# Kernel optimization log

Measured on AMD Instinct MI355X. Metric: run time of the kernel, lower is better.

## Reference

```python
import jax, jax.numpy as jnp
import numpy as np

B, S, D, H = 4, 2048, 1024, 16
HD = D // H
EPS = 1e-5


def setup_inputs() -> dict:
    key = jax.random.key(0)
    ks = jax.random.split(key, 12)
    scale = 1.0 / np.sqrt(D)
    inp = {
        "x": jax.random.normal(ks[0], (B, S, D), dtype=jnp.float32),
        "template_ids": jax.random.randint(ks[1], (B, S), 0, 1000, dtype=jnp.int64)
            if jax.config.jax_enable_x64 else jax.random.randint(ks[1], (B, S), 0, 1000, dtype=jnp.int32),
        "attention_mask": jnp.ones((B, S), dtype=jnp.int32),
        "Wq": jax.random.normal(ks[2], (D, D), dtype=jnp.float32) * scale,
        "bq": jnp.zeros((D,), dtype=jnp.float32),
        "Wk": jax.random.normal(ks[3], (D, D), dtype=jnp.float32) * scale,
        "bk": jnp.zeros((D,), dtype=jnp.float32),
        "Wv": jax.random.normal(ks[4], (D, D), dtype=jnp.float32) * scale,
        "bv": jnp.zeros((D,), dtype=jnp.float32),
        "Wo": jax.random.normal(ks[5], (D, D), dtype=jnp.float32) * scale,
        "bo": jnp.zeros((D,), dtype=jnp.float32),
        "gamma": jnp.ones((D,), dtype=jnp.float32),
        "beta": jnp.zeros((D,), dtype=jnp.float32),
    }
    return inp


def _split_heads(t):
    # [B,S,D] -> [B,H,S,HD]
    return t.reshape(B, S, H, HD).transpose(0, 2, 1, 3)


def reference(x, template_ids, attention_mask, Wq, bq, Wk, bk, Wv, bv, Wo, bo, gamma, beta):
    q = _split_heads(x @ Wq.T + bq)
    k = _split_heads(x @ Wk.T + bk)
    v = _split_heads(x @ Wv.T + bv)
    # [B,H,S,S]
    scores = jnp.einsum("bhqd,bhkd->bhqk", q, k) / jnp.sqrt(jnp.float32(HD))
    mask = attention_mask[:, None, None, :]  # broadcast over heads and query dim
    scores = jnp.where(mask == 0, jnp.float32(-10000.0), scores)
    attn = jax.nn.softmax(scores, axis=-1)  # dropout is identity in eval
    out = jnp.einsum("bhqk,bhkd->bhqd", attn, v)
    out = out.transpose(0, 2, 1, 3).reshape(B, S, D)
    out = out @ Wo.T + bo
    # residual + LayerNorm
    y = x + out
    mu = jnp.mean(y, axis=-1, keepdims=True)
    var = jnp.var(y, axis=-1, keepdims=True)
    return (y - mu) * jax.lax.rsqrt(var + EPS) * gamma + beta
```

## Files before the change

kernel.cpp:

```cpp
#include <hip/hip_runtime.h>

typedef unsigned short u16;
typedef unsigned int u32;
typedef __attribute__((ext_vector_type(8))) short bf16x8;
typedef __attribute__((ext_vector_type(4))) float f32x4;

#define NB 4
#define SS 2048
#define DD 1024
#define NH 16
#define HD 64
#define MM (NB*SS)

struct __align__(16) Pack16 { unsigned int w0, w1, w2, w3; };
union PU { Pack16 p; u16 s[8]; };

__device__ __forceinline__ float b2f(u16 u) {
    union { unsigned int i; float f; } v; v.i = ((unsigned int)u) << 16; return v.f;
}
__device__ __forceinline__ u16 f2b(float f) {
    union { unsigned int i; float f; } v; v.f = f;
    return (u16)((v.i + 0x7FFFu + ((v.i >> 16) & 1u)) >> 16);
}
__device__ __forceinline__ float rdS(const void* p, size_t i, int mode) {
    return mode ? ((const float*)p)[i] : b2f(((const u16*)p)[i]);
}
__device__ __forceinline__ float ex2(float x) { return __builtin_amdgcn_exp2f(x); }
__device__ __forceinline__ u32 cvtpk(float lo, float hi) {
    u32 r;
    asm("v_cvt_pk_bf16_f32 %0, %1, %2" : "=v"(r) : "v"(lo), "v"(hi));
    return r;
}

__device__ __forceinline__ void cp16(const u16* g, u16* l) {
    __builtin_amdgcn_global_load_lds(
        (const __attribute__((address_space(1))) void*)g,
        (__attribute__((address_space(3))) void*)l, 16, 0, 0);
}

__device__ __forceinline__ void pl32swap(u32& a, u32& b) {
    asm volatile("v_permlane32_swap_b32 %0, %1" : "+v"(a), "+v"(b));
}
__device__ __forceinline__ void pl16swap(u32& a, u32& b) {
    asm volatile("v_permlane16_swap_b32 %0, %1" : "+v"(a), "+v"(b));
}

#define QSC 0.1803368801111204f
#define GX ((size_t)MM * DD / 8)
#define GW ((size_t)DD * DD / 8)
#define GTOT (GX + 4 * GW + 512)

__global__ __launch_bounds__(256) void convert_kernel(
    const void* __restrict__ x,
    const void* __restrict__ Wq, const void* __restrict__ Wk,
    const void* __restrict__ Wv, const void* __restrict__ Wo,
    const void* __restrict__ bq, const void* __restrict__ bk,
    const void* __restrict__ bv, const void* __restrict__ bo,
    u16* __restrict__ xb, u16* __restrict__ Wc, u16* __restrict__ Wob,
    u16* __restrict__ bcat, const u32* __restrict__ gamma_w)
{
    const int mode = (gamma_w[0] == 0x3F800000u) ? 1 : 0;
    size_t g = (size_t)blockIdx.x * 256 + threadIdx.x;
    const void* src; u16* dst; size_t off; float sc = 1.0f;
    if (g < GX)               { src = x;  dst = xb;              off = g * 8; }
    else if (g < GX + GW)     { src = Wq; dst = Wc;              off = (g - GX) * 8; sc = QSC; }
    else if (g < GX + 2 * GW) { src = Wk; dst = Wc + (size_t)DD * DD;     off = (g - GX - GW) * 8; }
    else if (g < GX + 3 * GW) { src = Wv; dst = Wc + (size_t)2 * DD * DD; off = (g - GX - 2 * GW) * 8; }
    else if (g < GX + 4 * GW) { src = Wo; dst = Wob;             off = (g - GX - 3 * GW) * 8; }
    else {
        size_t gg = g - (GX + 4 * GW);
        int which = (int)(gg >> 7); off = (gg & 127) * 8;
        src = (which == 0) ? bq : (which == 1) ? bk : (which == 2) ? bv : bo;
        dst = bcat + which * DD;
        if (which == 0) sc = QSC;
    }
    PU o;
    if (mode) {
        const float* s = (const float*)src + off;
        float4 a = ((const float4*)s)[0];
        float4 b = ((const float4*)s)[1];
        o.s[0] = f2b(a.x * sc); o.s[1] = f2b(a.y * sc);
        o.s[2] = f2b(a.z * sc); o.s[3] = f2b(a.w * sc);
        o.s[4] = f2b(b.x * sc); o.s[5] = f2b(b.y * sc);
        o.s[6] = f2b(b.z * sc); o.s[7] = f2b(b.w * sc);
    } else {
        PU in; in.p = *(const Pack16*)((const u16*)src + off);
#pragma unroll
        for (int j = 0; j < 8; j++) o.s[j] = f2b(b2f(in.s[j]) * sc);
    }
    *(Pack16*)(dst + off) = o.p;
}

__global__ __launch_bounds__(256) void gemm_qkv(
    const u16* __restrict__ xb, const u16* __restrict__ Wc, const u16* __restrict__ bcat,
    u16* __restrict__ Q, u16* __restrict__ K, u16* __restrict__ V)
{
    __shared__ __align__(16) u16 sh[2 * 128 * 64];
    u16* As = sh;
    u16* Bs = sh + 128 * 64;

    const int lin = blockIdx.x;
    const int xcd = lin & 7;
    const int loc = lin >> 3;
    const int m0 = (xcd * 8 + (loc & 7)) * 128;
    const int n0 = (loc >> 3) * 128;

    const int tid  = threadIdx.x;
    const int wv   = tid >> 6;
    const int lane = tid & 63;
    const int wy = wv >> 1, wx = wv & 1;
    const int l15 = lane & 15, quad = lane >> 4;
    const int srow = lane >> 3;
    const int sw   = ((lane & 7) ^ srow) * 8;
    const int key  = l15 & 7;

    f32x4 acc[4][4];
#pragma unroll
    for (int i = 0; i < 4; i++)
#pragma unroll
        for (int j = 0; j < 4; j++) acc[i][j] = (f32x4){0.f, 0.f, 0.f, 0.f};

    for (int k0 = 0; k0 < DD; k0 += 64) {
#pragma unroll
        for (int c = 0; c < 4; c++) {
            cp16(&xb[(size_t)(m0 + wv * 32 + c * 8 + srow) * DD + k0 + sw],
                 &As[wv * 2048 + c * 512]);
            cp16(&Wc[(size_t)(n0 + wv * 32 + c * 8 + srow) * DD + k0 + sw],
                 &Bs[wv * 2048 + c * 512]);
        }
        __syncthreads();
#pragma unroll
        for (int ks = 0; ks < 2; ks++) {
            bf16x8 a[4], bb[4];
#pragma unroll
            for (int mt = 0; mt < 4; mt++)
                a[mt] = *(const bf16x8*)&As[(wy * 64 + mt * 16 + l15) * 64 +
                                            (((ks << 2) + quad) ^ key) * 8];
#pragma unroll
            for (int nt = 0; nt < 4; nt++)
                bb[nt] = *(const bf16x8*)&Bs[(wx * 64 + nt * 16 + l15) * 64 +
                                             (((ks << 2) + quad) ^ key) * 8];
#pragma unroll
            for (int mt = 0; mt < 4; mt++)
#pragma unroll
                for (int nt = 0; nt < 4; nt++)
                    acc[mt][nt] = __builtin_amdgcn_mfma_f32_16x16x32_bf16(
                        a[mt], bb[nt], acc[mt][nt], 0, 0, 0);
        }
        __syncthreads();
    }

    const int z = n0 >> 10;
    if (z != 2) {
        u16* out = (z == 0) ? Q : K;
#pragma unroll
        for (int nt = 0; nt < 4; nt++) {
            int n_g = n0 + wx * 64 + nt * 16 + l15;
            float bv_ = b2f(bcat[n_g]);
            int nn = n_g & 1023;
            int h = nn >> 6, hd = nn & 63;
#pragma unroll
            for (int mt = 0; mt < 4; mt++) {
#pragma unroll
                for (int r = 0; r < 4; r++) {
                    int m_g = m0 + wy * 64 + mt * 16 + quad * 4 + r;
                    int b = m_g >> 11, s = m_g & (SS - 1);
                    out[(((size_t)(b * NH + h) * SS) + s) * HD + hd] =
                        f2b(acc[mt][nt][r] + bv_);
                }
            }
        }
    } else {
        const int bb_ = m0 >> 11, sbase = m0 & (SS - 1);
#pragma unroll
        for (int ph = 0; ph < 2; ph++) {
            if (wx == ph) {
#pragma unroll
                for (int nt = 0; nt < 4; nt++) {
                    int n_loc = nt * 16 + l15;
                    float bv_ = b2f(bcat[n0 + ph * 64 + n_loc]);
#pragma unroll
                    for (int mt = 0; mt < 4; mt++) {
                        int m = wy * 64 + mt * 16 + quad * 4;
                        uint2 wr;
                        wr.x = (u32)f2b(acc[mt][nt][0] + bv_) |
                               ((u32)f2b(acc[mt][nt][1] + bv_) << 16);
                        wr.y = (u32)f2b(acc[mt][nt][2] + bv_) |
                               ((u32)f2b(acc[mt][nt][3] + bv_) << 16);
                        *(uint2*)&sh[n_loc * 136 + m] = wr;
                    }
                }
            }
            __syncthreads();
            {
                int row = tid >> 2;
                int sg  = tid & 3;
                int n_g = n0 + ph * 64 + row;
                int nn = n_g & 1023;
                int h = nn >> 6, hd = nn & 63;
                u16* dst = &V[(((size_t)(bb_ * NH + h)) * HD + hd) * SS + sbase];
#pragma unroll
                for (int j = 0; j < 4; j++) {
                    int mloc = sg * 32 + j * 8;
                    *(Pack16*)&dst[mloc] = *(const Pack16*)&sh[row * 136 + mloc];
                }
            }
            __syncthreads();
        }
    }
}

__global__ __launch_bounds__(256, 4) void attn_kernel(
    const u16* __restrict__ Q, const u16* __restrict__ K, const u16* __restrict__ V,
    const int* __restrict__ mask, u16* __restrict__ O)
{
    const int lin  = blockIdx.x;
    const int slot = lin >> 3;
    const int bh   = (lin & 7) * 8 + (slot >> 4);
    const int b = bh >> 4, h = bh & 15;
    const int q0 = (slot & 15) * 128;
    const u16* Qp  = Q + (size_t)bh * SS * HD;
    const u16* Kp  = K + (size_t)bh * SS * HD;
    const u16* Vtg = V + (size_t)bh * HD * SS;
    const int* mk = mask + b * SS;

    __shared__ __align__(16) u16 Kl[2 * 64 * 64];
    __shared__ __align__(16) u16 Vt[2 * 64 * 64];
    __shared__ int s_anymask;

    const int tid  = threadIdx.x;
    const int w    = tid >> 6;
    const int lane = tid & 63;
    const int l15 = lane & 15, quad = lane >> 4;
    const int srow = lane >> 3;
    const int sw   = ((lane & 7) ^ srow) * 8;
    const int key  = l15 & 7;

    if (tid == 0) s_anymask = 0;
    __syncthreads();
    {
        int local = 0;
#pragma unroll
        for (int i = 0; i < 2; i++) {
            int4 m4 = ((const int4*)mk)[i * 256 + tid];
            if ((m4.x == 0) | (m4.y == 0) | (m4.z == 0) | (m4.w == 0)) local = 1;
        }
        if (local) s_anymask = 1;
    }
    __syncthreads();
    const bool anymask = (s_anymask != 0);

    bf16x8 qf[2][2];
#pragma unroll
    for (int qt = 0; qt < 2; qt++)
#pragma unroll
        for (int ks = 0; ks < 2; ks++)
            qf[qt][ks] = *(const bf16x8*)&Qp[(size_t)(q0 + w * 32 + qt * 16 + l15) * HD +
                                             ks * 32 + quad * 8];

    bf16x8 onesf;
#pragma unroll
    for (int i = 0; i < 8; i++) onesf[i] = (short)0x3F80;

    f32x4 oacc[2][4];
#pragma unroll
    for (int i = 0; i < 2; i++)
#pragma unroll
        for (int j = 0; j < 4; j++) oacc[i][j] = (f32x4){0.f, 0.f, 0.f, 0.f};
    f32x4 sumacc[2];
#pragma unroll
    for (int i = 0; i < 2; i++) sumacc[i] = (f32x4){0.f, 0.f, 0.f, 0.f};

#pragma unroll
    for (int c = 0; c < 2; c++) {
        cp16(&Kp[(size_t)(w * 16 + c * 8 + srow) * HD + sw], &Kl[w * 1024 + c * 512]);
        cp16(&Vtg[(size_t)(w * 16 + c * 8 + srow) * SS + sw], &Vt[w * 1024 + c * 512]);
    }

    for (int it = 0; it < SS / 64; it++) {
        const int kv0 = it * 64;
        const int p = it & 1;
        __syncthreads();

        if (it + 1 < SS / 64) {
            const int kn = kv0 + 64;
#pragma unroll
            for (int c = 0; c < 2; c++) {
                cp16(&Kp[(size_t)(kn + w * 16 + c * 8 + srow) * HD + sw],
                     &Kl[(p ^ 1) * 4096 + w * 1024 + c * 512]);
                cp16(&Vtg[(size_t)(w * 16 + c * 8 + srow) * SS + kn + sw],
                     &Vt[(p ^ 1) * 4096 + w * 1024 + c * 512]);
            }
        }

        f32x4 sacc[4][2];
#pragma unroll
        for (int i = 0; i < 4; i++)
#pragma unroll
            for (int j = 0; j < 2; j++) sacc[i][j] = (f32x4){0.f, 0.f, 0.f, 0.f};
#pragma unroll
        for (int ks = 0; ks < 2; ks++) {
            bf16x8 kf[4];
#pragma unroll
            for (int kvt = 0; kvt < 4; kvt++)
                kf[kvt] = *(const bf16x8*)&Kl[p * 4096 + (kvt * 16 + l15) * 64 +
                                              (((ks << 2) + quad) ^ key) * 8];
            __builtin_amdgcn_s_setprio(1);
#pragma unroll
            for (int kvt = 0; kvt < 4; kvt++)
#pragma unroll
                for (int qt = 0; qt < 2; qt++)
                    sacc[kvt][qt] = __builtin_amdgcn_mfma_f32_16x16x32_bf16(
                        kf[kvt], qf[qt][ks], sacc[kvt][qt], 0, 0, 0);
            __builtin_amdgcn_s_setprio(0);
        }

        union { bf16x8 v; u32 d[4]; } paf[2][2];
#pragma unroll
        for (int qt = 0; qt < 2; qt++) {
            u32 pk[4][2];
#pragma unroll
            for (int kvt = 0; kvt < 4; kvt++) {
                f32x4 vv = sacc[kvt][qt];
                if (anymask) {
#pragma unroll
                    for (int r = 0; r < 4; r++) {
                        int kv = kv0 + kvt * 16 + quad * 4 + r;
                        if (mk[kv] == 0) vv[r] = -20000.0f;
                    }
                }
                pk[kvt][0] = cvtpk(ex2(vv[0]), ex2(vv[1]));
                pk[kvt][1] = cvtpk(ex2(vv[2]), ex2(vv[3]));
            }
#pragma unroll
            for (int ks2 = 0; ks2 < 2; ks2++) {
#pragma unroll
                for (int c = 0; c < 2; c++) {
                    u32 x0 = pk[ks2 * 2 + 0][c];
                    u32 x1 = pk[ks2 * 2 + 1][c];
                    pl32swap(x0, x1);
                    pl16swap(x0, x1);
                    paf[qt][ks2].d[c]     = x0;
                    paf[qt][ks2].d[2 + c] = x1;
                }
            }
        }

#pragma unroll
        for (int ks2 = 0; ks2 < 2; ks2++) {
            bf16x8 vf[4];
#pragma unroll
            for (int nt = 0; nt < 4; nt++)
                vf[nt] = *(const bf16x8*)&Vt[p * 4096 + (nt * 16 + l15) * 64 +
                                             (((ks2 << 2) + quad) ^ key) * 8];
            __builtin_amdgcn_s_setprio(1);
#pragma unroll
            for (int qt = 0; qt < 2; qt++) {
#pragma unroll
                for (int nt = 0; nt < 4; nt++)
                    oacc[qt][nt] = __builtin_amdgcn_mfma_f32_16x16x32_bf16(
                        paf[qt][ks2].v, vf[nt], oacc[qt][nt], 0, 0, 0);
                sumacc[qt] = __builtin_amdgcn_mfma_f32_16x16x32_bf16(
                    paf[qt][ks2].v, onesf, sumacc[qt], 0, 0, 0);
            }
            __builtin_amdgcn_s_setprio(0);
        }
    }

#pragma unroll
    for (int qt = 0; qt < 2; qt++) {
#pragma unroll
        for (int r = 0; r < 4; r++) {
            float inv = 1.0f / sumacc[qt][r];
            int row = q0 + w * 32 + qt * 16 + quad * 4 + r;
            size_t base = ((size_t)(b * SS + row)) * DD + h * HD;
#pragma unroll
            for (int nt = 0; nt < 4; nt++)
                O[base + nt * 16 + l15] = f2b(oacc[qt][nt][r] * inv);
        }
    }
}

__global__ __launch_bounds__(256) void gemm_oproj(
    const u16* __restrict__ A, const u16* __restrict__ Wob, const u16* __restrict__ bcat,
    u16* __restrict__ Y0, u16* __restrict__ Y1)
{
    __shared__ __align__(16) u16 As[128 * 64];
    __shared__ __align__(16) u16 Bs[128 * 64];

    const int lin = blockIdx.x;
    const int xcd = lin & 7;
    const int loc = lin >> 3;
    const int kz  = loc >> 6;
    const int r_  = loc & 63;
    const int m0 = (xcd * 8 + (r_ & 7)) * 128;
    const int n0 = (r_ >> 3) * 128;
    const int kbase = kz * (DD / 2);

    const int tid  = threadIdx.x;
    const int wv   = tid >> 6;
    const int lane = tid & 63;
    const int wy = wv >> 1, wx = wv & 1;
    const int l15 = lane & 15, quad = lane >> 4;
    const int srow = lane >> 3;
    const int sw   = ((lane & 7) ^ srow) * 8;
    const int key  = l15 & 7;

    f32x4 acc[4][4];
#pragma unroll
    for (int i = 0; i < 4; i++)
#pragma unroll
        for (int j = 0; j < 4; j++) acc[i][j] = (f32x4){0.f, 0.f, 0.f, 0.f};

    for (int k0 = 0; k0 < DD / 2; k0 += 64) {
#pragma unroll
        for (int c = 0; c < 4; c++) {
            cp16(&A[(size_t)(m0 + wv * 32 + c * 8 + srow) * DD + kbase + k0 + sw],
                 &As[wv * 2048 + c * 512]);
            cp16(&Wob[(size_t)(n0 + wv * 32 + c * 8 + srow) * DD + kbase + k0 + sw],
                 &Bs[wv * 2048 + c * 512]);
        }
        __syncthreads();
#pragma unroll
        for (int ks = 0; ks < 2; ks++) {
            bf16x8 a[4], bb[4];
#pragma unroll
            for (int mt = 0; mt < 4; mt++)
                a[mt] = *(const bf16x8*)&As[(wy * 64 + mt * 16 + l15) * 64 +
                                            (((ks << 2) + quad) ^ key) * 8];
#pragma unroll
            for (int nt = 0; nt < 4; nt++)
                bb[nt] = *(const bf16x8*)&Bs[(wx * 64 + nt * 16 + l15) * 64 +
                                             (((ks << 2) + quad) ^ key) * 8];
#pragma unroll
            for (int mt = 0; mt < 4; mt++)
#pragma unroll
                for (int nt = 0; nt < 4; nt++)
                    acc[mt][nt] = __builtin_amdgcn_mfma_f32_16x16x32_bf16(
                        a[mt], bb[nt], acc[mt][nt], 0, 0, 0);
        }
        __syncthreads();
    }

    u16* Y = kz ? Y1 : Y0;
#pragma unroll
    for (int nt = 0; nt < 4; nt++) {
        int n_g = n0 + wx * 64 + nt * 16 + l15;
        float bv_ = kz ? 0.f : b2f(bcat[3 * DD + n_g]);
#pragma unroll
        for (int mt = 0; mt < 4; mt++) {
#pragma unroll
            for (int r = 0; r < 4; r++) {
                int m_g = m0 + wy * 64 + mt * 16 + quad * 4 + r;
                Y[(size_t)m_g * DD + n_g] = f2b(acc[mt][nt][r] + bv_);
            }
        }
    }
}

__global__ __launch_bounds__(256) void ln_kernel(
    const u16* __restrict__ Y0p, const u16* __restrict__ Y1p,
    const void* __restrict__ x,
    const void* __restrict__ gamma, const void* __restrict__ beta,
    void* __restrict__ out)
{
    const int mode = (((const u32*)gamma)[0] == 0x3F800000u) ? 1 : 0;
    const int w    = threadIdx.x >> 6;
    const int lane = threadIdx.x & 63;
    const int row  = blockIdx.x * 4 + w;
    const u16* y0 = Y0p + (size_t)row * DD;
    const u16* y1 = Y1p + (size_t)row * DD;

    float vals[16];
    float s = 0.f, sq = 0.f;
#pragma unroll
    for (int i = 0; i < 2; i++) {
        PU d0; d0.p = *(const Pack16*)&y0[i * 512 + lane * 8];
        PU d1; d1.p = *(const Pack16*)&y1[i * 512 + lane * 8];
        if (mode) {
            const float* xp = (const float*)x + (size_t)row * DD + i * 512 + lane * 8;
            float4 xa = ((const float4*)xp)[0];
            float4 xb2 = ((const float4*)xp)[1];
            float xr[8] = {xa.x, xa.y, xa.z, xa.w, xb2.x, xb2.y, xb2.z, xb2.w};
#pragma unroll
            for (int j = 0; j < 8; j++) {
                float f = b2f(d0.s[j]) + b2f(d1.s[j]) + xr[j];
                vals[i * 8 + j] = f;
                s += f; sq += f * f;
            }
        } else {
            const u16* xp = (const u16*)x + (size_t)row * DD + i * 512 + lane * 8;
            PU xd; xd.p = *(const Pack16*)xp;
#pragma unroll
            for (int j = 0; j < 8; j++) {
                float f = b2f(d0.s[j]) + b2f(d1.s[j]) + b2f(xd.s[j]);
                vals[i * 8 + j] = f;
                s += f; sq += f * f;
            }
        }
    }
#pragma unroll
    for (int off = 1; off < 64; off <<= 1) {
        s  += __shfl_xor(s, off);
        sq += __shfl_xor(sq, off);
    }
    float mu  = s * (1.0f / 1024.0f);
    float var = sq * (1.0f / 1024.0f) - mu * mu;
    float rs  = rsqrtf(var + 1e-5f);

#pragma unroll
    for (int i = 0; i < 2; i++) {
        float r8[8];
#pragma unroll
        for (int j = 0; j < 8; j++) {
            int col = i * 512 + lane * 8 + j;
            r8[j] = (vals[i * 8 + j] - mu) * rs * rdS(gamma, col, mode) + rdS(beta, col, mode);
        }
        if (mode) {
            float* of = (float*)out + (size_t)row * DD + i * 512 + lane * 8;
            ((float4*)of)[0] = make_float4(r8[0], r8[1], r8[2], r8[3]);
            ((float4*)of)[1] = make_float4(r8[4], r8[5], r8[6], r8[7]);
        } else {
            PU ob;
#pragma unroll
            for (int j = 0; j < 8; j++) ob.s[j] = f2b(r8[j]);
            *(Pack16*)((u16*)out + (size_t)row * DD + i * 512 + lane * 8) = ob.p;
        }
    }
}

extern "C" void kernel_launch(void* const* d_in, const int* in_sizes, int n_in,
                              void* d_out, int out_size, void* d_ws, size_t ws_size,
                              hipStream_t stream)
{
    const void* x     = d_in[0];
    const int* mask   = (const int*)d_in[2];
    const void* Wq    = d_in[3];
    const void* bq    = d_in[4];
    const void* Wk    = d_in[5];
    const void* bk    = d_in[6];
    const void* Wv    = d_in[7];
    const void* bv    = d_in[8];
    const void* Wo    = d_in[9];
    const void* bo    = d_in[10];
    const void* gamma = d_in[11];
    const void* beta  = d_in[12];

    const size_t n = (size_t)MM * DD;
    u16* xb   = (u16*)((char*)d_ws + 256);
    u16* Wc   = xb + n;
    u16* Wob  = Wc + (size_t)3 * DD * DD;
    u16* bcat = Wob + (size_t)DD * DD;
    u16* Qb   = bcat + 4096;
    u16* Kb   = Qb + n;
    u16* Vb   = Kb + n;
    u16* Ab   = Vb + n;

    convert_kernel<<<(unsigned)(GTOT / 256), 256, 0, stream>>>(
        x, Wq, Wk, Wv, Wo, bq, bk, bv, bo, xb, Wc, Wob, bcat, (const u32*)gamma);
    gemm_qkv<<<1536, 256, 0, stream>>>(xb, Wc, bcat, Qb, Kb, Vb);
    attn_kernel<<<1024, 256, 0, stream>>>(Qb, Kb, Vb, mask, Ab);
    gemm_oproj<<<1024, 256, 0, stream>>>(Ab, Wob, bcat, Qb, Kb);
    ln_kernel<<<MM / 4, 256, 0, stream>>>(Qb, Kb, x, gamma, beta, d_out);
}
```

Measured before the change: 317.9 us.

## Stage Q/K and O-proj epilogues through LDS for coalesced 16-byte stores

The Q/K projection epilogue and the output-projection epilogue now write bf16 results into shared memory first, then each thread copies contiguous 64-byte row segments to global memory with 16-byte stores. Before, each lane issued scattered 2-byte stores. The attention kernel's QK^T loop is unrolled by hand so the first MFMA starts from a zero constant instead of a separately zeroed accumulator. The epilogues add two barriers per phase and reuse the GEMM tile LDS as a staging buffer.

```diff
diff --git a/kernel.cpp b/kernel.cpp
--- a/kernel.cpp
+++ b/kernel.cpp
@@ -151,27 +151,41 @@
     }
 
     const int z = n0 >> 10;
+    const int bbk = m0 >> 11, sbase = m0 & (SS - 1);
     if (z != 2) {
         u16* out = (z == 0) ? Q : K;
-#pragma unroll
-        for (int nt = 0; nt < 4; nt++) {
-            int n_g = n0 + wx * 64 + nt * 16 + l15;
-            float bv_ = b2f(bcat[n_g]);
-            int nn = n_g & 1023;
-            int h = nn >> 6, hd = nn & 63;
-#pragma unroll
-            for (int mt = 0; mt < 4; mt++) {
-#pragma unroll
-                for (int r = 0; r < 4; r++) {
-                    int m_g = m0 + wy * 64 + mt * 16 + quad * 4 + r;
-                    int b = m_g >> 11, s = m_g & (SS - 1);
-                    out[(((size_t)(b * NH + h) * SS) + s) * HD + hd] =
-                        f2b(acc[mt][nt][r] + bv_);
+        const int nn0h = (n0 & 1023) >> 6;
+#pragma unroll
+        for (int ph = 0; ph < 2; ph++) {
+            if (wx == ph) {
+#pragma unroll
+                for (int nt = 0; nt < 4; nt++) {
+                    int n_loc = nt * 16 + l15;
+                    float bv_ = b2f(bcat[n0 + ph * 64 + n_loc]);
+#pragma unroll
+                    for (int mt = 0; mt < 4; mt++) {
+#pragma unroll
+                        for (int r = 0; r < 4; r++) {
+                            int m = wy * 64 + mt * 16 + quad * 4 + r;
+                            sh[m * 72 + n_loc] = f2b(acc[mt][nt][r] + bv_);
+                        }
+                    }
                 }
             }
+            __syncthreads();
+            {
+                int m = tid >> 1, half = tid & 1;
+                int h = nn0h + ph;
+                u16* drow = out + (((size_t)(bbk * NH + h)) * SS + sbase + m) * HD +
+                            half * 32;
+                const u16* srow_ = &sh[m * 72 + half * 32];
+#pragma unroll
+                for (int j = 0; j < 4; j++)
+                    *(Pack16*)&drow[j * 8] = *(const Pack16*)&srow_[j * 8];
+            }
+            __syncthreads();
         }
     } else {
-        const int bb_ = m0 >> 11, sbase = m0 & (SS - 1);
 #pragma unroll
         for (int ph = 0; ph < 2; ph++) {
             if (wx == ph) {
@@ -198,7 +212,7 @@
                 int n_g = n0 + ph * 64 + row;
                 int nn = n_g & 1023;
                 int h = nn >> 6, hd = nn & 63;
-                u16* dst = &V[(((size_t)(bb_ * NH + h)) * HD + hd) * SS + sbase];
+                u16* dst = &V[(((size_t)(bbk * NH + h)) * HD + hd) * SS + sbase];
 #pragma unroll
                 for (int j = 0; j < 4; j++) {
                     int mloc = sg * 32 + j * 8;
@@ -271,6 +285,8 @@
 #pragma unroll
     for (int i = 0; i < 2; i++) sumacc[i] = (f32x4){0.f, 0.f, 0.f, 0.f};
 
+    const f32x4 fz = (f32x4){0.f, 0.f, 0.f, 0.f};
+
 #pragma unroll
     for (int c = 0; c < 2; c++) {
         cp16(&Kp[(size_t)(w * 16 + c * 8 + srow) * HD + sw], &Kl[w * 1024 + c * 512]);
@@ -294,24 +310,31 @@
         }
 
         f32x4 sacc[4][2];
-#pragma unroll
-        for (int i = 0; i < 4; i++)
-#pragma unroll
-            for (int j = 0; j < 2; j++) sacc[i][j] = (f32x4){0.f, 0.f, 0.f, 0.f};
-#pragma unroll
-        for (int ks = 0; ks < 2; ks++) {
+        {
             bf16x8 kf[4];
 #pragma unroll
             for (int kvt = 0; kvt < 4; kvt++)
                 kf[kvt] = *(const bf16x8*)&Kl[p * 4096 + (kvt * 16 + l15) * 64 +
-                                              (((ks << 2) + quad) ^ key) * 8];
+                                              (quad ^ key) * 8];
             __builtin_amdgcn_s_setprio(1);
 #pragma unroll
             for (int kvt = 0; kvt < 4; kvt++)
 #pragma unroll
                 for (int qt = 0; qt < 2; qt++)
                     sacc[kvt][qt] = __builtin_amdgcn_mfma_f32_16x16x32_bf16(
-                        kf[kvt], qf[qt][ks], sacc[kvt][qt], 0, 0, 0);
+                        kf[kvt], qf[qt][0], fz, 0, 0, 0);
+            __builtin_amdgcn_s_setprio(0);
+#pragma unroll
+            for (int kvt = 0; kvt < 4; kvt++)
+                kf[kvt] = *(const bf16x8*)&Kl[p * 4096 + (kvt * 16 + l15) * 64 +
+                                              ((4 + quad) ^ key) * 8];
+            __builtin_amdgcn_s_setprio(1);
+#pragma unroll
+            for (int kvt = 0; kvt < 4; kvt++)
+#pragma unroll
+                for (int qt = 0; qt < 2; qt++)
+                    sacc[kvt][qt] = __builtin_amdgcn_mfma_f32_16x16x32_bf16(
+                        kf[kvt], qf[qt][1], sacc[kvt][qt], 0, 0, 0);
             __builtin_amdgcn_s_setprio(0);
         }
 
@@ -352,7 +375,7 @@
 #pragma unroll
             for (int nt = 0; nt < 4; nt++)
                 vf[nt] = *(const bf16x8*)&Vt[p * 4096 + (nt * 16 + l15) * 64 +
-                                             (((ks2 << 2) + quad) ^ key) * 8];
+                                             (((ks2 << 1) * 2 + quad) ^ key) * 8];
             __builtin_amdgcn_s_setprio(1);
 #pragma unroll
             for (int qt = 0; qt < 2; qt++) {
@@ -385,8 +408,9 @@
     const u16* __restrict__ A, const u16* __restrict__ Wob, const u16* __restrict__ bcat,
     u16* __restrict__ Y0, u16* __restrict__ Y1)
 {
-    __shared__ __align__(16) u16 As[128 * 64];
-    __shared__ __align__(16) u16 Bs[128 * 64];
+    __shared__ __align__(16) u16 sh[2 * 128 * 64];
+    u16* As = sh;
+    u16* Bs = sh + 128 * 64;
 
     const int lin = blockIdx.x;
     const int xcd = lin & 7;
@@ -444,17 +468,32 @@
 
     u16* Y = kz ? Y1 : Y0;
 #pragma unroll
-    for (int nt = 0; nt < 4; nt++) {
-        int n_g = n0 + wx * 64 + nt * 16 + l15;
-        float bv_ = kz ? 0.f : b2f(bcat[3 * DD + n_g]);
-#pragma unroll
-        for (int mt = 0; mt < 4; mt++) {
-#pragma unroll
-            for (int r = 0; r < 4; r++) {
-                int m_g = m0 + wy * 64 + mt * 16 + quad * 4 + r;
-                Y[(size_t)m_g * DD + n_g] = f2b(acc[mt][nt][r] + bv_);
-            }
-        }
+    for (int ph = 0; ph < 2; ph++) {
+        if (wx == ph) {
+#pragma unroll
+            for (int nt = 0; nt < 4; nt++) {
+                int n_loc = nt * 16 + l15;
+                float bv_ = kz ? 0.f : b2f(bcat[3 * DD + n0 + ph * 64 + n_loc]);
+#pragma unroll
+                for (int mt = 0; mt < 4; mt++) {
+#pragma unroll
+                    for (int r = 0; r < 4; r++) {
+                        int m = wy * 64 + mt * 16 + quad * 4 + r;
+                        sh[m * 72 + n_loc] = f2b(acc[mt][nt][r] + bv_);
+                    }
+                }
+            }
+        }
+        __syncthreads();
+        {
+            int m = tid >> 1, half = tid & 1;
+            u16* drow = Y + (size_t)(m0 + m) * DD + n0 + ph * 64 + half * 32;
+            const u16* srow_ = &sh[m * 72 + half * 32];
+#pragma unroll
+            for (int j = 0; j < 4; j++)
+                *(Pack16*)&drow[j * 8] = *(const Pack16*)&srow_[j * 8];
+        }
+        __syncthreads();
     }
 }
 
```

After: 340.5 us. 1.07x slower.
